# Performance work log

Measured on AMD Instinct MI355X. Metric: run time of the kernel, lower is better.

## Reference

```python
import jax, jax.numpy as jnp
from jax import lax
import numpy as np

B, S, D_IN = 2048, 512, 5
H, E_DIM, N_EMB, C_CONV = 64, 32, 64, 32
COMMIT = 0.01


def _lstm_params(key, in_dim, hid):
    ks = jax.random.split(key, 4)
    sc = 1.0 / np.sqrt(hid)
    wih = jax.random.uniform(ks[0], (4 * hid, in_dim), minval=-sc, maxval=sc)
    whh = jax.random.uniform(ks[1], (4 * hid, hid), minval=-sc, maxval=sc)
    bih = jax.random.uniform(ks[2], (4 * hid,), minval=-sc, maxval=sc)
    bhh = jax.random.uniform(ks[3], (4 * hid,), minval=-sc, maxval=sc)
    return wih, whh, bih, bhh


def setup_inputs() -> dict:
    key = jax.random.key(0)
    ks = jax.random.split(key, 12)
    inp = {}
    inp['x'] = jax.random.normal(ks[0], (B, S, D_IN), dtype=jnp.float32)
    inp['conv_w'] = jax.random.normal(ks[1], (C_CONV, D_IN, 3)) * 0.2  # OIH
    inp['conv_b'] = jax.random.normal(ks[2], (C_CONV,)) * 0.05
    inp['bn_g'] = jnp.ones((C_CONV,)) + jax.random.normal(ks[3], (C_CONV,)) * 0.05
    inp['bn_b'] = jax.random.normal(ks[4], (C_CONV,)) * 0.05
    inp['bn_m'] = jax.random.normal(ks[5], (C_CONV,)) * 0.1
    inp['bn_v'] = jax.random.uniform(ks[6], (C_CONV,), minval=0.5, maxval=1.5)
    cw = _lstm_params(ks[7], C_CONV, H)
    cw1 = _lstm_params(jax.random.fold_in(ks[7], 1), H, H)
    vw = _lstm_params(ks[8], D_IN, H)
    vw1 = _lstm_params(jax.random.fold_in(ks[8], 1), H, H)
    for pre, p in (('cnn0', cw), ('cnn1', cw1), ('vq0', vw), ('vq1', vw1)):
        inp[pre + '_wih'], inp[pre + '_whh'], inp[pre + '_bih'], inp[pre + '_bhh'] = p
    inp['proj_w'] = jax.random.normal(ks[9], (E_DIM, H)) * (1.0 / np.sqrt(H))
    inp['proj_b'] = jax.random.normal(ks[10], (E_DIM,)) * 0.05
    xav = np.sqrt(6.0 / (N_EMB + E_DIM))
    inp['codebook'] = jax.random.uniform(ks[11], (N_EMB, E_DIM), minval=-xav, maxval=xav)
    return inp


def _lstm_layer(xs, wih, whh, bih, bhh):
    # xs: [S, B, in] -> (ys [S,B,H], h_final [B,H])
    b = xs.shape[1]
    h0 = jnp.zeros((b, H), xs.dtype)
    bias = bih + bhh

    def step(carry, x_t):
        h, c = carry
        gates = x_t @ wih.T + h @ whh.T + bias
        i, f, g, o = jnp.split(gates, 4, axis=-1)
        c = jax.nn.sigmoid(f) * c + jax.nn.sigmoid(i) * jnp.tanh(g)
        h = jax.nn.sigmoid(o) * jnp.tanh(c)
        return (h, c), h

    (h, c), ys = lax.scan(step, (h0, h0), xs)
    return ys, h


def _forward(x, conv_w, conv_b, bn_g, bn_b, bn_m, bn_v,
             cnn0_wih, cnn0_whh, cnn0_bih, cnn0_bhh,
             cnn1_wih, cnn1_whh, cnn1_bih, cnn1_bhh,
             vq0_wih, vq0_whh, vq0_bih, vq0_bhh,
             vq1_wih, vq1_whh, vq1_bih, vq1_bhh,
             proj_w, proj_b, codebook):
    # CNN stream: conv1d(k=3, pad=1) + BN (eval) + ReLU; dropout = identity (eval)
    x_ncw = jnp.transpose(x, (0, 2, 1))  # [B, D_IN, S]
    y = lax.conv_general_dilated(x_ncw, conv_w, (1,), [(1, 1)],
                                 dimension_numbers=('NCH', 'OIH', 'NCH'))
    y = y + conv_b[None, :, None]
    y = (y - bn_m[None, :, None]) * (bn_g / jnp.sqrt(bn_v + 1e-5))[None, :, None] + bn_b[None, :, None]
    y = jax.nn.relu(y)
    y = jnp.transpose(y, (2, 0, 1))  # [S, B, 32] time-major
    ys, _ = _lstm_layer(y, cnn0_wih, cnn0_whh, cnn0_bih, cnn0_bhh)
    _, cnn_features = _lstm_layer(ys, cnn1_wih, cnn1_whh, cnn1_bih, cnn1_bhh)  # [B, H]

    # VQ stream
    xt = jnp.transpose(x, (1, 0, 2))  # [S, B, D_IN]
    ys2, _ = _lstm_layer(xt, vq0_wih, vq0_whh, vq0_bih, vq0_bhh)
    _, vq_hidden = _lstm_layer(ys2, vq1_wih, vq1_whh, vq1_bih, vq1_bhh)  # [B, H]
    vq_proj = vq_hidden @ proj_w.T + proj_b  # [B, E_DIM]

    # Vector quantization
    d = (jnp.sum(vq_proj ** 2, axis=1, keepdims=True)
         + jnp.sum(codebook ** 2, axis=1)
         - 2.0 * vq_proj @ codebook.T)  # [B, N_EMB]
    idx = jnp.argmin(d, axis=1)
    quantized = codebook[idx]  # [B, E_DIM]
    e_loss = jnp.mean((lax.stop_gradient(quantized) - vq_proj) ** 2)
    q_loss = jnp.mean((quantized - lax.stop_gradient(vq_proj)) ** 2)
    vq_loss = q_loss + COMMIT * e_loss
    quantized = vq_proj + lax.stop_gradient(quantized - vq_proj)  # STE
    enc = jax.nn.one_hot(idx, N_EMB, dtype=vq_proj.dtype)
    avg_probs = jnp.mean(enc, axis=0)
    perplexity = jnp.exp(-jnp.sum(avg_probs * jnp.log(avg_probs + 1e-10)))

    combined = jnp.concatenate([cnn_features, quantized], axis=1)  # [B, H+E_DIM]
    return combined, vq_loss, perplexity


def reference(x, conv_w, conv_b, bn_g, bn_b, bn_m, bn_v,
              cnn0_wih, cnn0_whh, cnn0_bih, cnn0_bhh,
              cnn1_wih, cnn1_whh, cnn1_bih, cnn1_bhh,
              vq0_wih, vq0_whh, vq0_bih, vq0_bhh,
              vq1_wih, vq1_whh, vq1_bih, vq1_bhh,
              proj_w, proj_b, codebook):
    combined, vq_loss, perplexity = _forward(
        x, conv_w, conv_b, bn_g, bn_b, bn_m, bn_v,
        cnn0_wih, cnn0_whh, cnn0_bih, cnn0_bhh,
        cnn1_wih, cnn1_whh, cnn1_bih, cnn1_bhh,
        vq0_wih, vq0_whh, vq0_bih, vq0_bhh,
        vq1_wih, vq1_whh, vq1_bih, vq1_bhh,
        proj_w, proj_b, codebook)
    # num_classes=None -> returns (combined, combined, vq_loss, perplexity)
    return combined, combined, vq_loss, perplexity
```

## Files before the change

### kernel.cpp

```cpp
#include <hip/hip_runtime.h>
#include <math.h>
#include <stdint.h>

#define B_TOT 2048
#define SEQ   512
#define DIN   5
#define HID   64
#define EDIM  32
#define NEMB  64
#define BT    16
#define NBLK_STREAM 128
#define COMB  96
#define OUTC  (B_TOT*COMB)

typedef __attribute__((ext_vector_type(8))) _Float16 half8;
typedef __attribute__((ext_vector_type(4))) _Float16 half4;
typedef __attribute__((ext_vector_type(4))) float float4v;

#if __has_builtin(__builtin_amdgcn_exp2f)
#define FEXP2(x) __builtin_amdgcn_exp2f(x)
#else
#define FEXP2(x) exp2f(x)
#endif
#if __has_builtin(__builtin_amdgcn_rcpf)
#define FRCP(x) __builtin_amdgcn_rcpf(x)
#else
#define FRCP(x) (1.0f/(x))
#endif

#define L2E  1.44269504089f
#define L2E2 2.88539008178f

__device__ __forceinline__ float sig_b(float a, float bp){
  return FRCP(1.0f + FEXP2(fmaf(a, -L2E, bp)));
}
__device__ __forceinline__ float tanh_b(float a, float bp){
  return fmaf(2.0f, FRCP(1.0f + FEXP2(fmaf(a, -L2E2, bp))), -1.0f);
}
__device__ __forceinline__ float ftanh(float x){
  return fmaf(2.0f, FRCP(1.0f + FEXP2(-L2E2 * x)), -1.0f);
}
__device__ __forceinline__ float fsig(float x){
  return FRCP(1.0f + FEXP2(-L2E * x));
}
#define MFMA16(a,b,c) __builtin_amdgcn_mfma_f32_16x16x32_f16((a),(b),(c),0,0,0)

#define LOOP_BARRIER() do { \
    asm volatile("s_waitcnt lgkmcnt(0)" ::: "memory"); \
    __builtin_amdgcn_s_barrier(); \
  } while (0)

__global__ __launch_bounds__(256)
void conv_pre_kernel(const float* __restrict__ xg,
                     const float* __restrict__ conv_w, const float* __restrict__ conv_b,
                     const float* __restrict__ bn_g, const float* __restrict__ bn_b,
                     const float* __restrict__ bn_m, const float* __restrict__ bn_v,
                     _Float16* __restrict__ Y,
                     float* __restrict__ ws_f, int* __restrict__ ws_hist,
                     int* __restrict__ ws_cnt)
{
  const int tid = threadIdx.x;
  if (blockIdx.x == 0) {
    if (tid == 0) ws_f[0] = 0.f;
    if (tid < NEMB) ws_hist[tid] = 0;
    if (tid == 64) ws_cnt[0] = 0;
  }
  const int cg = tid & 7;
  const int it = tid >> 3;
  float wv[4][15], bz[4];
#pragma unroll
  for (int j = 0; j < 4; ++j) {
    const int ch = cg*4 + j;
    const float s = bn_g[ch] * rsqrtf(bn_v[ch] + 1e-5f);
#pragma unroll
    for (int i = 0; i < 5; ++i)
#pragma unroll
      for (int tau = 0; tau < 3; ++tau)
        wv[j][tau*5 + i] = conv_w[ch*15 + i*3 + tau] * s;
    bz[j] = (conv_b[ch] - bn_m[ch]) * s + bn_b[ch];
  }
  const int ngrp = (B_TOT * SEQ) / 32;
  for (int grp = blockIdx.x; grp < ngrp; grp += gridDim.x) {
    const int idx = grp*32 + it;
    const int t = idx & (SEQ-1);
    const float* xb = xg + (size_t)idx*DIN;
    float xm[5], x0[5], xp[5];
#pragma unroll
    for (int i = 0; i < 5; ++i) {
      x0[i] = xb[i];
      xm[i] = (t > 0)     ? xb[i - DIN] : 0.f;
      xp[i] = (t < SEQ-1) ? xb[i + DIN] : 0.f;
    }
    half4 yv;
#pragma unroll
    for (int j = 0; j < 4; ++j) {
      float s = bz[j];
#pragma unroll
      for (int i = 0; i < 5; ++i)
        s += wv[j][i]*xm[i] + wv[j][5+i]*x0[i] + wv[j][10+i]*xp[i];
      yv[j] = (_Float16)fmaxf(s, 0.f);
    }
    *(half4*)(Y + (size_t)idx*32 + cg*4) = yv;
  }
}

template<bool PRE>
__global__ __launch_bounds__(1024)
__attribute__((amdgpu_waves_per_eu(4, 4)))
void fused_kernel(const float* __restrict__ xg,
                  const float* __restrict__ conv_w, const float* __restrict__ conv_b,
                  const float* __restrict__ bn_g, const float* __restrict__ bn_b,
                  const float* __restrict__ bn_m, const float* __restrict__ bn_v,
                  const float* __restrict__ cnn0_wih, const float* __restrict__ cnn0_whh,
                  const float* __restrict__ cnn0_bih, const float* __restrict__ cnn0_bhh,
                  const float* __restrict__ cnn1_wih, const float* __restrict__ cnn1_whh,
                  const float* __restrict__ cnn1_bih, const float* __restrict__ cnn1_bhh,
                  const float* __restrict__ vq0_wih, const float* __restrict__ vq0_whh,
                  const float* __restrict__ vq0_bih, const float* __restrict__ vq0_bhh,
                  const float* __restrict__ vq1_wih, const float* __restrict__ vq1_whh,
                  const float* __restrict__ vq1_bih, const float* __restrict__ vq1_bhh,
                  const float* __restrict__ proj_w, const float* __restrict__ proj_b,
                  const float* __restrict__ codebook, const _Float16* __restrict__ Yg,
                  float* __restrict__ out, float* __restrict__ ws_f,
                  int* __restrict__ ws_hist, int* __restrict__ ws_cnt)
{
  __shared__ __align__(16) _Float16 ZT[2][5][4][BT][8];
  __shared__ __align__(16) float hfin[BT][HID];
  __shared__ __align__(16) float pbuf[BT][EDIM];
  __shared__ float xwin[4][BT][DIN];

  const int tid  = threadIdx.x;
  const bool is_cnn = (blockIdx.x < NBLK_STREAM);
  const int b0   = (is_cnn ? blockIdx.x : blockIdx.x - NBLK_STREAM) * BT;
  const int w    = tid >> 6;
  const int lane = tid & 63;
  const int n16  = lane & 15;
  const int quad = lane >> 4;
  const int u    = 4*w + quad;

  const float* wih0 = is_cnn ? cnn0_wih : vq0_wih;
  const float* whh0 = is_cnn ? cnn0_whh : vq0_whh;
  const float* bih0 = is_cnn ? cnn0_bih : vq0_bih;
  const float* bhh0 = is_cnn ? cnn0_bhh : vq0_bhh;
  const float* wih1 = is_cnn ? cnn1_wih : vq1_wih;
  const float* whh1 = is_cnn ? cnn1_whh : vq1_whh;
  const float* bih1 = is_cnn ? cnn1_bih : vq1_bih;
  const float* bhh1 = is_cnn ? cnn1_bhh : vq1_bhh;

  const int orow = 64*(n16 & 3) + 4*w + (n16 >> 2);
  half8 Ah0[3], Ah1[4];
#pragma unroll
  for (int kt = 0; kt < 3; ++kt) {
    half8 vh;
#pragma unroll
    for (int j = 0; j < 8; ++j) {
      const int g = kt*32 + quad*8 + j;
      float wv;
      if (is_cnn) wv = (g < 32) ? wih0[orow*32 + g] : whh0[orow*64 + (g-32)];
      else        wv = (g < 5) ? wih0[orow*5 + g] : (g < 32 ? 0.f : whh0[orow*64 + (g-32)]);
      vh[j] = (_Float16)wv;
    }
    Ah0[kt] = vh;
  }
#pragma unroll
  for (int kt = 0; kt < 4; ++kt) {
    half8 vh;
#pragma unroll
    for (int j = 0; j < 8; ++j) {
      const int g = kt*32 + quad*8 + j;
      float wv = (g < 64) ? wih1[orow*64 + g] : whh1[orow*64 + (g-64)];
      vh[j] = (_Float16)wv;
    }
    Ah1[kt] = vh;
  }

  float bp0[4], bp1[4];
#pragma unroll
  for (int r = 0; r < 4; ++r) {
    const float k = (r == 2) ? L2E2 : L2E;
    bp0[r] = -k * (bih0[64*r + u] + bhh0[64*r + u]);
    bp1[r] = -k * (bih1[64*r + u] + bhh1[64*r + u]);
  }
  const float4v zero4 = {0.f, 0.f, 0.f, 0.f};

  float wr[16];
  if (!PRE) {
#pragma unroll
    for (int i = 0; i < 16; ++i) wr[i] = 0.f;
    if (is_cnn && tid < 512) {
      const int cc = tid >> 4;
      float s = bn_g[cc] * rsqrtf(bn_v[cc] + 1e-5f);
#pragma unroll
      for (int i = 0; i < 5; ++i)
#pragma unroll
        for (int tau = 0; tau < 3; ++tau)
          wr[tau*5 + i] = conv_w[cc*15 + i*3 + tau] * s;
      wr[15] = (conv_b[cc] - bn_m[cc]) * s + bn_b[cc];
    }
  }

  for (int i2 = tid; i2 < 2*5*4*BT*8/2; i2 += 1024) ((uint32_t*)ZT)[i2] = 0;

  const int xn = tid / 5, xi = tid % 5;
  const int yn = tid >> 2, ykg = tid & 3;
  float xpref = 0.f;
  half8 ypref{};
  const _Float16* Yb = nullptr;
  if (PRE && is_cnn && tid < 64)
    Yb = Yg + ((size_t)(b0 + yn)*SEQ)*32 + ykg*8;

  #define ZB(b) ((_Float16*)(&ZT[(b)][0][0][0][0]))
  #define ZIDX(tile,k32,n) (((tile)*4 + (((k32)>>3)&3))*(BT*8) + (n)*8 + ((k32)&7))

  if (!PRE && is_cnn) {
    if (tid < BT*DIN) {
#pragma unroll
      for (int j = 0; j < 4; ++j)
        xwin[j][xn][xi] = xg[((size_t)(b0+xn)*SEQ + j)*DIN + xi];
    }
  }
  __syncthreads();

  if (is_cnn) {
    if (PRE) {
      if (tid < 64) {
        half8 y0 = *(const half8*)(Yb + (size_t)0*32);
        half8 y1 = *(const half8*)(Yb + (size_t)1*32);
        ypref    = *(const half8*)(Yb + (size_t)2*32);
        *(half8*)&ZB(1)[ykg*(BT*8) + yn*8] = y0;
        *(half8*)&ZB(0)[ykg*(BT*8) + yn*8] = y1;
      }
    } else {
      if (tid < 512) {
        const int cc = tid >> 4, cn = tid & 15;
        float s = wr[15];
#pragma unroll
        for (int i = 0; i < 5; ++i)
          s += wr[5+i]*xwin[0][cn][i] + wr[10+i]*xwin[1][cn][i];
        s = fmaxf(s, 0.f);
        ZB(1)[ZIDX(0, cc, cn)] = (_Float16)s;
      }
    }
  } else {
    if (tid < BT*DIN) {
      float x0v = xg[((size_t)(b0+xn)*SEQ + 0)*DIN + xi];
      float x1v = xg[((size_t)(b0+xn)*SEQ + 1)*DIN + xi];
      ZB(1)[ZIDX(0, xi, xn)] = (_Float16)x0v;
      ZB(0)[ZIDX(0, xi, xn)] = (_Float16)x1v;
      xpref = xg[((size_t)(b0+xn)*SEQ + 2)*DIN + xi];
    }
  }
  __syncthreads();

  float c0 = 0.f, c1 = 0.f, h1v = 0.f;
  {
    half8 bt0 = *(const half8*)&ZT[1][0][quad][n16][0];
    half8 bt1 = *(const half8*)&ZT[1][1][quad][n16][0];
    half8 bt2 = *(const half8*)&ZT[1][2][quad][n16][0];
    float4v a0 = MFMA16(Ah0[0], bt0, zero4);
    a0 = MFMA16(Ah0[1], bt1, a0);
    a0 = MFMA16(Ah0[2], bt2, a0);
    float i0 = sig_b(a0[0], bp0[0]);
    float g0 = tanh_b(a0[2], bp0[2]);
    float o0 = sig_b(a0[3], bp0[3]);
    c0 = i0 * g0;
    float h0 = o0 * ftanh(c0);
    ZB(0)[ZIDX(1 + (u>>5), u & 31, n16)] = (_Float16)h0;
  }
  if (!PRE && is_cnn) {
    if (tid < 512) {
      const int cc = tid >> 4, cn = tid & 15;
      float s = wr[15];
#pragma unroll
      for (int i = 0; i < 5; ++i)
        s += wr[i]*xwin[0][cn][i] + wr[5+i]*xwin[1][cn][i]
           + wr[10+i]*xwin[2][cn][i];
      s = fmaxf(s, 0.f);
      ZB(0)[ZIDX(0, cc, cn)] = (_Float16)s;
    }
    if (tid < BT*DIN) xpref = xg[((size_t)(b0+xn)*SEQ + 4)*DIN + xi];
  }
  __syncthreads();

#pragma unroll 2
  for (int t = 0; t < SEQ; ++t) {
    const int rb = t & 1, wrb = rb ^ 1;
    half8 bt0 = *(const half8*)&ZT[rb][0][quad][n16][0];
    half8 bt1 = *(const half8*)&ZT[rb][1][quad][n16][0];
    half8 bt2 = *(const half8*)&ZT[rb][2][quad][n16][0];
    half8 bt3 = *(const half8*)&ZT[rb][3][quad][n16][0];
    half8 bt4 = *(const half8*)&ZT[rb][4][quad][n16][0];
    float4v p1 = MFMA16(Ah1[0], bt1, zero4);
    float4v q1 = MFMA16(Ah1[1], bt2, zero4);
    float4v p0 = MFMA16(Ah0[0], bt0, zero4);
    p1 = MFMA16(Ah1[2], bt3, p1);
    q1 = MFMA16(Ah1[3], bt4, q1);
    p0 = MFMA16(Ah0[1], bt1, p0);
    p0 = MFMA16(Ah0[2], bt2, p0);

    __builtin_amdgcn_s_setprio(1);
    {
      float a1i = p1[0] + q1[0], a1f = p1[1] + q1[1];
      float a1g = p1[2] + q1[2], a1o = p1[3] + q1[3];
      float i1 = sig_b(a1i, bp1[0]);
      float f1 = sig_b(a1f, bp1[1]);
      float g1 = tanh_b(a1g, bp1[2]);
      float o1 = sig_b(a1o, bp1[3]);
      c1 = fmaf(f1, c1, i1 * g1);
      float h1 = o1 * ftanh(c1);
      ZB(wrb)[ZIDX(3 + (u>>5), u & 31, n16)] = (_Float16)h1;
      if (is_cnn) h1v = h1;
      else if (t == SEQ-1) hfin[n16][u] = h1;
    }
    {
      float i0 = sig_b(p0[0], bp0[0]);
      float f0 = sig_b(p0[1], bp0[1]);
      float g0 = tanh_b(p0[2], bp0[2]);
      float o0 = sig_b(p0[3], bp0[3]);
      c0 = fmaf(f0, c0, i0 * g0);
      float h0 = o0 * ftanh(c0);
      ZB(wrb)[ZIDX(1 + (u>>5), u & 31, n16)] = (_Float16)h0;
    }
    if (is_cnn) {
      if (PRE) {
        if (tid < 64) {
          *(half8*)&ZB(wrb)[ykg*(BT*8) + yn*8] = ypref;
          const int tq = t + 3;
          if (tq < SEQ) ypref = *(const half8*)(Yb + (size_t)tq*32);
        }
      } else {
        if (tid < 512) {
          const int cc = tid >> 4, cn = tid & 15;
          const int s1 = (t+1)&3, s2 = (t+2)&3, s3 = (t+3)&3;
          float s = wr[15];
#pragma unroll
          for (int i = 0; i < 5; ++i)
            s += wr[i]*xwin[s1][cn][i] + wr[5+i]*xwin[s2][cn][i]
               + wr[10+i]*xwin[s3][cn][i];
          s = fmaxf(s, 0.f);
          ZB(wrb)[ZIDX(0, cc, cn)] = (_Float16)s;
        }
        if (tid < BT*DIN) {
          xwin[t & 3][xn][xi] = xpref;
          const int tq = t + 5;
          xpref = (tq < SEQ) ? xg[((size_t)(b0+xn)*SEQ + tq)*DIN + xi] : 0.f;
        }
      }
    } else {
      if (tid < BT*DIN) {
        ZB(wrb)[ZIDX(0, xi, xn)] = (_Float16)xpref;
        const int tq = t + 3;
        xpref = (tq < SEQ) ? xg[((size_t)(b0+xn)*SEQ + tq)*DIN + xi] : 0.f;
      }
    }
    __builtin_amdgcn_s_setprio(0);
    LOOP_BARRIER();
  }

  if (is_cnn) {
    const size_t gb = (size_t)(b0 + n16);
    out[gb*COMB + u]        = h1v;
    out[OUTC + gb*COMB + u] = h1v;
  } else {
    if (tid < 512) {
      const int pn = tid >> 5, pe = tid & 31;
      float s = proj_b[pe];
      const float* pw = proj_w + pe*HID;
#pragma unroll
      for (int k = 0; k < HID; ++k) s += hfin[pn][k] * pw[k];
      pbuf[pn][pe] = s;
    }
    __syncthreads();
    {
      const int bb = w;
      const int nn = lane;
      const float* cbn = codebook + nn*EDIM;
      float d = 0.f;
#pragma unroll
      for (int k = 0; k < EDIM; ++k) { float df = pbuf[bb][k] - cbn[k]; d += df*df; }
      int bi = nn;
#pragma unroll
      for (int off = 32; off > 0; off >>= 1) {
        float od = __shfl_down(d, off, 64);
        int   oi = __shfl_down(bi, off, 64);
        if (od < d || (od == d && oi < bi)) { d = od; bi = oi; }
      }
      bi = __shfl(bi, 0, 64);
      float lv = 0.f;
      if (nn < EDIM) {
        float q = codebook[bi*EDIM + nn];
        const size_t gb = (size_t)(b0 + bb);
        out[gb*COMB + HID + nn]        = q;
        out[OUTC + gb*COMB + HID + nn] = q;
        float df = q - pbuf[bb][nn];
        lv = df*df;
      }
#pragma unroll
      for (int off = 32; off > 0; off >>= 1) lv += __shfl_down(lv, off, 64);
      if (nn == 0) { atomicAdd(ws_f, lv); atomicAdd(&ws_hist[bi], 1); }
    }
    if (w == 0) {
      __threadfence();
      int c = 0;
      if (lane == 0) c = atomicAdd(ws_cnt, 1);
      c = __shfl(c, 0, 64);
      if (c == NBLK_STREAM - 1) {
        __threadfence();
        int hv = atomicAdd(&ws_hist[lane], 0);
        float p = (float)hv * (1.0f / (float)B_TOT);
        float e = -p * logf(p + 1e-10f);
#pragma unroll
        for (int off = 32; off > 0; off >>= 1) e += __shfl_down(e, off, 64);
        if (lane == 0) {
          float wf = atomicAdd(ws_f, 0.0f);
          float mse = wf * (1.0f / (float)(B_TOT * EDIM));
          out[2*OUTC + 0] = mse * 1.01f;
          out[2*OUTC + 1] = expf(e);
        }
      }
    }
  }
}

__global__ void zero_ws_kernel(float* ws_f, int* ws_hist, int* ws_cnt) {
  const int t = threadIdx.x;
  if (t == 0) ws_f[0] = 0.f;
  if (t < NEMB) ws_hist[t] = 0;
  if (t == 64) ws_cnt[0] = 0;
}

extern "C" void kernel_launch(void* const* d_in, const int* in_sizes, int n_in,
                              void* d_out, int out_size, void* d_ws, size_t ws_size,
                              hipStream_t stream) {
  const float* x        = (const float*)d_in[0];
  const float* conv_w   = (const float*)d_in[1];
  const float* conv_b   = (const float*)d_in[2];
  const float* bn_g     = (const float*)d_in[3];
  const float* bn_b     = (const float*)d_in[4];
  const float* bn_m     = (const float*)d_in[5];
  const float* bn_v     = (const float*)d_in[6];
  const float* cnn0_wih = (const float*)d_in[7];
  const float* cnn0_whh = (const float*)d_in[8];
  const float* cnn0_bih = (const float*)d_in[9];
  const float* cnn0_bhh = (const float*)d_in[10];
  const float* cnn1_wih = (const float*)d_in[11];
  const float* cnn1_whh = (const float*)d_in[12];
  const float* cnn1_bih = (const float*)d_in[13];
  const float* cnn1_bhh = (const float*)d_in[14];
  const float* vq0_wih  = (const float*)d_in[15];
  const float* vq0_whh  = (const float*)d_in[16];
  const float* vq0_bih  = (const float*)d_in[17];
  const float* vq0_bhh  = (const float*)d_in[18];
  const float* vq1_wih  = (const float*)d_in[19];
  const float* vq1_whh  = (const float*)d_in[20];
  const float* vq1_bih  = (const float*)d_in[21];
  const float* vq1_bhh  = (const float*)d_in[22];
  const float* proj_w   = (const float*)d_in[23];
  const float* proj_b   = (const float*)d_in[24];
  const float* codebook = (const float*)d_in[25];

  float* out     = (float*)d_out;
  float* ws_f    = (float*)d_ws;
  int*   ws_hist = (int*)d_ws + 16;
  int*   ws_cnt  = (int*)d_ws + 88;

  const size_t Y_BYTES = (size_t)B_TOT * SEQ * 32 * sizeof(_Float16);
  _Float16* Yg = (_Float16*)((char*)d_ws + 1024);
  const bool use_pre = (ws_size >= 1024 + Y_BYTES);

  if (use_pre) {
    hipLaunchKernelGGL(conv_pre_kernel, dim3(2048), dim3(256), 0, stream,
                       x, conv_w, conv_b, bn_g, bn_b, bn_m, bn_v, Yg,
                       ws_f, ws_hist, ws_cnt);
    hipLaunchKernelGGL((fused_kernel<true>), dim3(2*NBLK_STREAM), dim3(1024), 0, stream,
                       x, conv_w, conv_b, bn_g, bn_b, bn_m, bn_v,
                       cnn0_wih, cnn0_whh, cnn0_bih, cnn0_bhh,
                       cnn1_wih, cnn1_whh, cnn1_bih, cnn1_bhh,
                       vq0_wih, vq0_whh, vq0_bih, vq0_bhh,
                       vq1_wih, vq1_whh, vq1_bih, vq1_bhh,
                       proj_w, proj_b, codebook, Yg, out, ws_f, ws_hist, ws_cnt);
  } else {
    hipLaunchKernelGGL(zero_ws_kernel, dim3(1), dim3(128), 0, stream, ws_f, ws_hist, ws_cnt);
    hipLaunchKernelGGL((fused_kernel<false>), dim3(2*NBLK_STREAM), dim3(1024), 0, stream,
                       x, conv_w, conv_b, bn_g, bn_b, bn_m, bn_v,
                       cnn0_wih, cnn0_whh, cnn0_bih, cnn0_bhh,
                       cnn1_wih, cnn1_whh, cnn1_bih, cnn1_bhh,
                       vq0_wih, vq0_whh, vq0_bih, vq0_bhh,
                       vq1_wih, vq1_whh, vq1_bih, vq1_bhh,
                       proj_w, proj_b, codebook, Yg, out, ws_f, ws_hist, ws_cnt);
  }
}
```

Baseline: 570.1 us.

## Halve LSTM block size so each wave computes two gate tiles

The fused LSTM kernel now runs 512 threads (8 waves) per block instead of 1024. Each wave holds weights for two M-tiles and computes two hidden-unit groups per step, with the MFMAs interleaved across tiles. The aim is a cheaper per-step barrier and more independent MFMA work per wave for latency hiding, at the cost of more registers per thread and more serial work per wave. The conv pre-kernel also stages a shared 34x5 input window so neighbouring timesteps are not re-read from global memory, which adds two block barriers per group.

Result: slower. 598.9 us (+5.1%).

```diff
diff --git a/kernel.cpp b/kernel.cpp
--- a/kernel.cpp
+++ b/kernel.cpp
@@ -40,9 +40,6 @@
 __device__ __forceinline__ float ftanh(float x){
   return fmaf(2.0f, FRCP(1.0f + FEXP2(-L2E2 * x)), -1.0f);
 }
-__device__ __forceinline__ float fsig(float x){
-  return FRCP(1.0f + FEXP2(-L2E * x));
-}
 #define MFMA16(a,b,c) __builtin_amdgcn_mfma_f32_16x16x32_f16((a),(b),(c),0,0,0)
 
 #define LOOP_BARRIER() do { \
@@ -59,6 +56,7 @@
                      float* __restrict__ ws_f, int* __restrict__ ws_hist,
                      int* __restrict__ ws_cnt)
 {
+  __shared__ float xs[34][5];
   const int tid = threadIdx.x;
   if (blockIdx.x == 0) {
     if (tid == 0) ws_f[0] = 0.f;
@@ -67,6 +65,7 @@
   }
   const int cg = tid & 7;
   const int it = tid >> 3;
+  const int lr = tid / 5, lc = tid % 5;
   float wv[4][15], bz[4];
 #pragma unroll
   for (int j = 0; j < 4; ++j) {
@@ -81,16 +80,18 @@
   }
   const int ngrp = (B_TOT * SEQ) / 32;
   for (int grp = blockIdx.x; grp < ngrp; grp += gridDim.x) {
-    const int idx = grp*32 + it;
-    const int t = idx & (SEQ-1);
-    const float* xb = xg + (size_t)idx*DIN;
-    float xm[5], x0[5], xp[5];
-#pragma unroll
-    for (int i = 0; i < 5; ++i) {
-      x0[i] = xb[i];
-      xm[i] = (t > 0)     ? xb[i - DIN] : 0.f;
-      xp[i] = (t < SEQ-1) ? xb[i + DIN] : 0.f;
-    }
+    const int base = grp * 32;
+    const int t0   = base & (SEQ-1);
+    if (tid < 170) {
+      float v = 0.f;
+      const bool pad = (lr == 0 && t0 == 0) || (lr == 33 && t0 == SEQ-32);
+      if (!pad) v = xg[(size_t)(base - 1 + lr)*DIN + lc];
+      xs[lr][lc] = v;
+    }
+    __syncthreads();
+    const float* xm = xs[it];
+    const float* x0 = xs[it+1];
+    const float* xp = xs[it+2];
     half4 yv;
 #pragma unroll
     for (int j = 0; j < 4; ++j) {
@@ -100,13 +101,14 @@
         s += wv[j][i]*xm[i] + wv[j][5+i]*x0[i] + wv[j][10+i]*xp[i];
       yv[j] = (_Float16)fmaxf(s, 0.f);
     }
-    *(half4*)(Y + (size_t)idx*32 + cg*4) = yv;
+    *(half4*)(Y + (size_t)(base + it)*32 + cg*4) = yv;
+    __syncthreads();
   }
 }
 
 template<bool PRE>
-__global__ __launch_bounds__(1024)
-__attribute__((amdgpu_waves_per_eu(4, 4)))
+__global__ __launch_bounds__(512)
+__attribute__((amdgpu_waves_per_eu(2, 2)))
 void fused_kernel(const float* __restrict__ xg,
                   const float* __restrict__ conv_w, const float* __restrict__ conv_b,
                   const float* __restrict__ bn_g, const float* __restrict__ bn_b,
@@ -136,7 +138,7 @@
   const int lane = tid & 63;
   const int n16  = lane & 15;
   const int quad = lane >> 4;
-  const int u    = 4*w + quad;
+  const int uA   = 4*w + quad;
 
   const float* wih0 = is_cnn ? cnn0_wih : vq0_wih;
   const float* whh0 = is_cnn ? cnn0_whh : vq0_whh;
@@ -147,39 +149,43 @@
   const float* bih1 = is_cnn ? cnn1_bih : vq1_bih;
   const float* bhh1 = is_cnn ? cnn1_bhh : vq1_bhh;
 
-  const int orow = 64*(n16 & 3) + 4*w + (n16 >> 2);
-  half8 Ah0[3], Ah1[4];
-#pragma unroll
-  for (int kt = 0; kt < 3; ++kt) {
-    half8 vh;
-#pragma unroll
-    for (int j = 0; j < 8; ++j) {
-      const int g = kt*32 + quad*8 + j;
-      float wv;
-      if (is_cnn) wv = (g < 32) ? wih0[orow*32 + g] : whh0[orow*64 + (g-32)];
-      else        wv = (g < 5) ? wih0[orow*5 + g] : (g < 32 ? 0.f : whh0[orow*64 + (g-32)]);
-      vh[j] = (_Float16)wv;
-    }
-    Ah0[kt] = vh;
-  }
-#pragma unroll
-  for (int kt = 0; kt < 4; ++kt) {
-    half8 vh;
-#pragma unroll
-    for (int j = 0; j < 8; ++j) {
-      const int g = kt*32 + quad*8 + j;
-      float wv = (g < 64) ? wih1[orow*64 + g] : whh1[orow*64 + (g-64)];
-      vh[j] = (_Float16)wv;
-    }
-    Ah1[kt] = vh;
-  }
-
-  float bp0[4], bp1[4];
-#pragma unroll
-  for (int r = 0; r < 4; ++r) {
-    const float k = (r == 2) ? L2E2 : L2E;
-    bp0[r] = -k * (bih0[64*r + u] + bhh0[64*r + u]);
-    bp1[r] = -k * (bih1[64*r + u] + bhh1[64*r + u]);
+  half8 Ah0[2][3], Ah1[2][4];
+  float bp0[2][4], bp1[2][4];
+#pragma unroll
+  for (int mt = 0; mt < 2; ++mt) {
+    const int wm = w + 8*mt;
+    const int orow = 64*(n16 & 3) + 4*wm + (n16 >> 2);
+#pragma unroll
+    for (int kt = 0; kt < 3; ++kt) {
+      half8 vh;
+#pragma unroll
+      for (int j = 0; j < 8; ++j) {
+        const int g = kt*32 + quad*8 + j;
+        float wvv;
+        if (is_cnn) wvv = (g < 32) ? wih0[orow*32 + g] : whh0[orow*64 + (g-32)];
+        else        wvv = (g < 5) ? wih0[orow*5 + g] : (g < 32 ? 0.f : whh0[orow*64 + (g-32)]);
+        vh[j] = (_Float16)wvv;
+      }
+      Ah0[mt][kt] = vh;
+    }
+#pragma unroll
+    for (int kt = 0; kt < 4; ++kt) {
+      half8 vh;
+#pragma unroll
+      for (int j = 0; j < 8; ++j) {
+        const int g = kt*32 + quad*8 + j;
+        float wvv = (g < 64) ? wih1[orow*64 + g] : whh1[orow*64 + (g-64)];
+        vh[j] = (_Float16)wvv;
+      }
+      Ah1[mt][kt] = vh;
+    }
+    const int u = uA + 32*mt;
+#pragma unroll
+    for (int r = 0; r < 4; ++r) {
+      const float k = (r == 2) ? L2E2 : L2E;
+      bp0[mt][r] = -k * (bih0[64*r + u] + bhh0[64*r + u]);
+      bp1[mt][r] = -k * (bih1[64*r + u] + bhh1[64*r + u]);
+    }
   }
   const float4v zero4 = {0.f, 0.f, 0.f, 0.f};
 
@@ -187,7 +193,7 @@
   if (!PRE) {
 #pragma unroll
     for (int i = 0; i < 16; ++i) wr[i] = 0.f;
-    if (is_cnn && tid < 512) {
+    if (is_cnn) {
       const int cc = tid >> 4;
       float s = bn_g[cc] * rsqrtf(bn_v[cc] + 1e-5f);
 #pragma unroll
@@ -199,7 +205,7 @@
     }
   }
 
-  for (int i2 = tid; i2 < 2*5*4*BT*8/2; i2 += 1024) ((uint32_t*)ZT)[i2] = 0;
+  for (int i2 = tid; i2 < 2*5*4*BT*8/2; i2 += 512) ((uint32_t*)ZT)[i2] = 0;
 
   const int xn = tid / 5, xi = tid % 5;
   const int yn = tid >> 2, ykg = tid & 3;
@@ -231,7 +237,7 @@
         *(half8*)&ZB(0)[ykg*(BT*8) + yn*8] = y1;
       }
     } else {
-      if (tid < 512) {
+      {
         const int cc = tid >> 4, cn = tid & 15;
         float s = wr[15];
 #pragma unroll
@@ -252,23 +258,26 @@
   }
   __syncthreads();
 
-  float c0 = 0.f, c1 = 0.f, h1v = 0.f;
+  float c0[2] = {0.f, 0.f}, c1[2] = {0.f, 0.f}, h1v[2] = {0.f, 0.f};
   {
     half8 bt0 = *(const half8*)&ZT[1][0][quad][n16][0];
     half8 bt1 = *(const half8*)&ZT[1][1][quad][n16][0];
     half8 bt2 = *(const half8*)&ZT[1][2][quad][n16][0];
-    float4v a0 = MFMA16(Ah0[0], bt0, zero4);
-    a0 = MFMA16(Ah0[1], bt1, a0);
-    a0 = MFMA16(Ah0[2], bt2, a0);
-    float i0 = sig_b(a0[0], bp0[0]);
-    float g0 = tanh_b(a0[2], bp0[2]);
-    float o0 = sig_b(a0[3], bp0[3]);
-    c0 = i0 * g0;
-    float h0 = o0 * ftanh(c0);
-    ZB(0)[ZIDX(1 + (u>>5), u & 31, n16)] = (_Float16)h0;
+#pragma unroll
+    for (int mt = 0; mt < 2; ++mt) {
+      float4v a0 = MFMA16(Ah0[mt][0], bt0, zero4);
+      a0 = MFMA16(Ah0[mt][1], bt1, a0);
+      a0 = MFMA16(Ah0[mt][2], bt2, a0);
+      float i0 = sig_b(a0[0], bp0[mt][0]);
+      float g0 = tanh_b(a0[2], bp0[mt][2]);
+      float o0 = sig_b(a0[3], bp0[mt][3]);
+      c0[mt] = i0 * g0;
+      float h0 = o0 * ftanh(c0[mt]);
+      ZB(0)[ZIDX(1 + mt, uA, n16)] = (_Float16)h0;
+    }
   }
   if (!PRE && is_cnn) {
-    if (tid < 512) {
+    {
       const int cc = tid >> 4, cn = tid & 15;
       float s = wr[15];
 #pragma unroll
@@ -290,36 +299,48 @@
     half8 bt2 = *(const half8*)&ZT[rb][2][quad][n16][0];
     half8 bt3 = *(const half8*)&ZT[rb][3][quad][n16][0];
     half8 bt4 = *(const half8*)&ZT[rb][4][quad][n16][0];
-    float4v p1 = MFMA16(Ah1[0], bt1, zero4);
-    float4v q1 = MFMA16(Ah1[1], bt2, zero4);
-    float4v p0 = MFMA16(Ah0[0], bt0, zero4);
-    p1 = MFMA16(Ah1[2], bt3, p1);
-    q1 = MFMA16(Ah1[3], bt4, q1);
-    p0 = MFMA16(Ah0[1], bt1, p0);
-    p0 = MFMA16(Ah0[2], bt2, p0);
+    float4v p1[2], q1[2], p0[2];
+#pragma unroll
+    for (int mt = 0; mt < 2; ++mt) {
+      p1[mt] = MFMA16(Ah1[mt][0], bt1, zero4);
+      q1[mt] = MFMA16(Ah1[mt][1], bt2, zero4);
+      p0[mt] = MFMA16(Ah0[mt][0], bt0, zero4);
+    }
+#pragma unroll
+    for (int mt = 0; mt < 2; ++mt) {
+      p1[mt] = MFMA16(Ah1[mt][2], bt3, p1[mt]);
+      q1[mt] = MFMA16(Ah1[mt][3], bt4, q1[mt]);
+      p0[mt] = MFMA16(Ah0[mt][1], bt1, p0[mt]);
+    }
+#pragma unroll
+    for (int mt = 0; mt < 2; ++mt)
+      p0[mt] = MFMA16(Ah0[mt][2], bt2, p0[mt]);
 
     __builtin_amdgcn_s_setprio(1);
-    {
-      float a1i = p1[0] + q1[0], a1f = p1[1] + q1[1];
-      float a1g = p1[2] + q1[2], a1o = p1[3] + q1[3];
-      float i1 = sig_b(a1i, bp1[0]);
-      float f1 = sig_b(a1f, bp1[1]);
-      float g1 = tanh_b(a1g, bp1[2]);
-      float o1 = sig_b(a1o, bp1[3]);
-      c1 = fmaf(f1, c1, i1 * g1);
-      float h1 = o1 * ftanh(c1);
-      ZB(wrb)[ZIDX(3 + (u>>5), u & 31, n16)] = (_Float16)h1;
-      if (is_cnn) h1v = h1;
-      else if (t == SEQ-1) hfin[n16][u] = h1;
-    }
-    {
-      float i0 = sig_b(p0[0], bp0[0]);
-      float f0 = sig_b(p0[1], bp0[1]);
-      float g0 = tanh_b(p0[2], bp0[2]);
-      float o0 = sig_b(p0[3], bp0[3]);
-      c0 = fmaf(f0, c0, i0 * g0);
-      float h0 = o0 * ftanh(c0);
-      ZB(wrb)[ZIDX(1 + (u>>5), u & 31, n16)] = (_Float16)h0;
+#pragma unroll
+    for (int mt = 0; mt < 2; ++mt) {
+      {
+        float a1i = p1[mt][0] + q1[mt][0], a1f = p1[mt][1] + q1[mt][1];
+        float a1g = p1[mt][2] + q1[mt][2], a1o = p1[mt][3] + q1[mt][3];
+        float i1 = sig_b(a1i, bp1[mt][0]);
+        float f1 = sig_b(a1f, bp1[mt][1]);
+        float g1 = tanh_b(a1g, bp1[mt][2]);
+        float o1 = sig_b(a1o, bp1[mt][3]);
+        c1[mt] = fmaf(f1, c1[mt], i1 * g1);
+        float h1 = o1 * ftanh(c1[mt]);
+        ZB(wrb)[ZIDX(3 + mt, uA, n16)] = (_Float16)h1;
+        if (is_cnn) h1v[mt] = h1;
+        else if (t == SEQ-1) hfin[n16][uA + 32*mt] = h1;
+      }
+      {
+        float i0 = sig_b(p0[mt][0], bp0[mt][0]);
+        float f0 = sig_b(p0[mt][1], bp0[mt][1]);
+        float g0 = tanh_b(p0[mt][2], bp0[mt][2]);
+        float o0 = sig_b(p0[mt][3], bp0[mt][3]);
+        c0[mt] = fmaf(f0, c0[mt], i0 * g0);
+        float h0 = o0 * ftanh(c0[mt]);
+        ZB(wrb)[ZIDX(1 + mt, uA, n16)] = (_Float16)h0;
+      }
     }
     if (is_cnn) {
       if (PRE) {
@@ -329,7 +350,7 @@
           if (tq < SEQ) ypref = *(const half8*)(Yb + (size_t)tq*32);
         }
       } else {
-        if (tid < 512) {
+        {
           const int cc = tid >> 4, cn = tid & 15;
           const int s1 = (t+1)&3, s2 = (t+2)&3, s3 = (t+3)&3;
           float s = wr[15];
@@ -359,10 +380,12 @@
 
   if (is_cnn) {
     const size_t gb = (size_t)(b0 + n16);
-    out[gb*COMB + u]        = h1v;
-    out[OUTC + gb*COMB + u] = h1v;
+    out[gb*COMB + uA]             = h1v[0];
+    out[OUTC + gb*COMB + uA]      = h1v[0];
+    out[gb*COMB + uA + 32]        = h1v[1];
+    out[OUTC + gb*COMB + uA + 32] = h1v[1];
   } else {
-    if (tid < 512) {
+    {
       const int pn = tid >> 5, pe = tid & 31;
       float s = proj_b[pe];
       const float* pw = proj_w + pe*HID;
@@ -371,8 +394,9 @@
       pbuf[pn][pe] = s;
     }
     __syncthreads();
-    {
-      const int bb = w;
+#pragma unroll
+    for (int hf = 0; hf < 2; ++hf) {
+      const int bb = w + 8*hf;
       const int nn = lane;
       const float* cbn = codebook + nn*EDIM;
       float d = 0.f;
@@ -472,7 +496,7 @@
     hipLaunchKernelGGL(conv_pre_kernel, dim3(2048), dim3(256), 0, stream,
                        x, conv_w, conv_b, bn_g, bn_b, bn_m, bn_v, Yg,
                        ws_f, ws_hist, ws_cnt);
-    hipLaunchKernelGGL((fused_kernel<true>), dim3(2*NBLK_STREAM), dim3(1024), 0, stream,
+    hipLaunchKernelGGL((fused_kernel<true>), dim3(2*NBLK_STREAM), dim3(512), 0, stream,
                        x, conv_w, conv_b, bn_g, bn_b, bn_m, bn_v,
                        cnn0_wih, cnn0_whh, cnn0_bih, cnn0_bhh,
                        cnn1_wih, cnn1_whh, cnn1_bih, cnn1_bhh,
@@ -481,7 +505,7 @@
                        proj_w, proj_b, codebook, Yg, out, ws_f, ws_hist, ws_cnt);
   } else {
     hipLaunchKernelGGL(zero_ws_kernel, dim3(1), dim3(128), 0, stream, ws_f, ws_hist, ws_cnt);
-    hipLaunchKernelGGL((fused_kernel<false>), dim3(2*NBLK_STREAM), dim3(1024), 0, stream,
+    hipLaunchKernelGGL((fused_kernel<false>), dim3(2*NBLK_STREAM), dim3(512), 0, stream,
                        x, conv_w, conv_b, bn_g, bn_b, bn_m, bn_v,
                        cnn0_wih, cnn0_whh, cnn0_bih, cnn0_bhh,
                        cnn1_wih, cnn1_whh, cnn1_bih, cnn1_bhh,
```
